# Kernel optimization log

Hardware: AMD Instinct MI355X
Metric: run time of the kernel (lower is better)

## Reference

```python
import jax, jax.numpy as jnp
import numpy as np

N, F, H, FO = 4096, 512, 4, 128  # nodes, in-feat, heads, out-feat per head
NEG_INF = -1e10
LRELU_ALPHA = 0.2


def setup_inputs() -> dict:
    key = jax.random.key(0)
    k_x, k_a, k_w, k_as, k_an = jax.random.split(key, 5)
    X = jax.random.normal(k_x, (N, F), dtype=jnp.float32)
    A = (jax.random.uniform(k_a, (N, N)) < 0.01).astype(jnp.float32)
    A = jnp.minimum(A + jnp.eye(N, dtype=jnp.float32), 1.0)
    W = jax.random.normal(k_w, (H, F, FO), dtype=jnp.float32) * 0.05       # per-head kernels
    b = jnp.zeros((H, FO), dtype=jnp.float32)                               # per-head biases
    a_self = jax.random.normal(k_as, (H, FO), dtype=jnp.float32) * 0.05    # attn_kernel_self (F_,1) per head
    a_neigh = jax.random.normal(k_an, (H, FO), dtype=jnp.float32) * 0.05   # attn_kernel_neigh (F_,1) per head
    return {"X": X, "A": A, "W": W, "b": b, "a_self": a_self, "a_neigh": a_neigh}


def reference(X, A, W, b, a_self, a_neigh):
    # features[h] = X @ W[h] -> [H, N, FO]
    feats = jnp.einsum('nf,hfo->hno', X, W)
    # Nx1 self / neighbor scores per head -> [H, N]
    e_s = jnp.einsum('hno,ho->hn', feats, a_self)
    e_n = jnp.einsum('hno,ho->hn', feats, a_neigh)
    # broadcast-add to [H, N, N], LeakyReLU(0.2), additive adjacency mask
    logits = e_s[:, :, None] + e_n[:, None, :]
    logits = jnp.where(logits > 0, logits, LRELU_ALPHA * logits)
    logits = logits + NEG_INF * (1.0 - A)[None, :, :]
    attn = jax.nn.softmax(logits, axis=-1)          # [H, N, N]
    out = jnp.einsum('hnm,hmo->hno', attn, feats)   # weighted aggregate
    out = out + b[:, None, :]
    # concat heads: [N, H*FO]
    out = jnp.transpose(out, (1, 0, 2)).reshape(X.shape[0], -1)
    return jax.nn.relu(out)
```

## Files before the change

kernel.cpp:

```cpp
#include <hip/hip_runtime.h>
#include <math.h>

#define NODES 4096
#define FIN   512
#define HEADS 4
#define FOUT  128
#define COLS  512

typedef short  short8  __attribute__((ext_vector_type(8)));
typedef float  floatx4 __attribute__((ext_vector_type(4)));

__device__ inline void split2(float x, short& hi, short& lo) {
    unsigned xb = __float_as_uint(x);
    unsigned hb = xb & 0xFFFF0000u;
    float hf = __uint_as_float(hb);
    float r  = x - hf;
    hi = (short)(hb >> 16);
    lo = (short)(__float_as_uint(r) >> 16);
}

__global__ __launch_bounds__(256) void convert_split(
    const float* __restrict__ X, const float* __restrict__ W,
    short* __restrict__ Xhi, short* __restrict__ Xlo,
    short* __restrict__ Wthi, short* __restrict__ Wtlo)
{
    int t = blockIdx.x * 256 + threadIdx.x;
    const int NX = NODES * FIN;
    const int stride = gridDim.x * 256;
    for (int i = t; i < NX; i += stride) {
        short hi, lo; split2(X[i], hi, lo);
        Xhi[i] = hi; Xlo[i] = lo;
    }
    const int NW = HEADS * FIN * FOUT;
    for (int i = t; i < NW; i += stride) {
        int h = i >> 16;
        int f = (i >> 7) & (FIN - 1);
        int o = i & (FOUT - 1);
        short hi, lo; split2(W[i], hi, lo);
        size_t dst = (size_t)(h * FOUT + o) * FIN + f;
        Wthi[dst] = hi; Wtlo[dst] = lo;
    }
}

__global__ __launch_bounds__(256) void gemm_mfma(
    const short* __restrict__ Xhi, const short* __restrict__ Xlo,
    const short* __restrict__ Bthi, const short* __restrict__ Btlo,
    float* __restrict__ feats)
{
    __shared__ short Ah[64][40], Al[64][40], Bh[64][40], Bl[64][40];
    const int tid = threadIdx.x;
    const int rowBase = blockIdx.y * 64;
    const int colBase = blockIdx.x * 64;
    const int lane = tid & 63, w = tid >> 6;
    const int quad = lane >> 4, lk = quad * 8, lm = lane & 15;

    floatx4 acc[4];
    #pragma unroll
    for (int mi = 0; mi < 4; mi++) acc[mi] = (floatx4)0.f;

    const int sr = tid >> 2;
    const int sk = (tid & 3) * 8;

    for (int k0 = 0; k0 < FIN; k0 += 32) {
        const float4 ah = *(const float4*)(Xhi  + (size_t)(rowBase + sr) * FIN + k0 + sk);
        const float4 al = *(const float4*)(Xlo  + (size_t)(rowBase + sr) * FIN + k0 + sk);
        const float4 bh = *(const float4*)(Bthi + (size_t)(colBase + sr) * FIN + k0 + sk);
        const float4 bl = *(const float4*)(Btlo + (size_t)(colBase + sr) * FIN + k0 + sk);
        __syncthreads();
        *(float4*)&Ah[sr][sk] = ah;
        *(float4*)&Al[sr][sk] = al;
        *(float4*)&Bh[sr][sk] = bh;
        *(float4*)&Bl[sr][sk] = bl;
        __syncthreads();

        short8 afh[4], afl[4];
        #pragma unroll
        for (int mi = 0; mi < 4; mi++) {
            afh[mi] = *(const short8*)&Ah[mi * 16 + lm][lk];
            afl[mi] = *(const short8*)&Al[mi * 16 + lm][lk];
        }
        short8 bfh = *(const short8*)&Bh[w * 16 + lm][lk];
        short8 bfl = *(const short8*)&Bl[w * 16 + lm][lk];
        #pragma unroll
        for (int mi = 0; mi < 4; mi++) {
            acc[mi] = __builtin_amdgcn_mfma_f32_16x16x32_bf16(afh[mi], bfh, acc[mi], 0, 0, 0);
            acc[mi] = __builtin_amdgcn_mfma_f32_16x16x32_bf16(afh[mi], bfl, acc[mi], 0, 0, 0);
            acc[mi] = __builtin_amdgcn_mfma_f32_16x16x32_bf16(afl[mi], bfh, acc[mi], 0, 0, 0);
        }
    }
    #pragma unroll
    for (int mi = 0; mi < 4; mi++) {
        #pragma unroll
        for (int r = 0; r < 4; r++) {
            int row = rowBase + mi * 16 + quad * 4 + r;
            int col = colBase + w * 16 + lm;
            feats[(size_t)row * COLS + col] = acc[mi][r];
        }
    }
}

__global__ __launch_bounds__(64) void scores(
    const float* __restrict__ feats, const float* __restrict__ a_self,
    const float* __restrict__ a_neigh, float* __restrict__ e_s, float* __restrict__ e_n)
{
    const int n = blockIdx.x;
    const int l = threadIdx.x;
    float ps[HEADS], pn[HEADS];
    #pragma unroll
    for (int hh = 0; hh < HEADS; hh++) {
        float x0 = feats[(size_t)n * COLS + hh * FOUT + l];
        float x1 = feats[(size_t)n * COLS + hh * FOUT + l + 64];
        ps[hh] = x0 * a_self[hh * FOUT + l]  + x1 * a_self[hh * FOUT + l + 64];
        pn[hh] = x0 * a_neigh[hh * FOUT + l] + x1 * a_neigh[hh * FOUT + l + 64];
    }
    #pragma unroll
    for (int off = 32; off > 0; off >>= 1) {
        #pragma unroll
        for (int hh = 0; hh < HEADS; hh++) {
            ps[hh] += __shfl_xor(ps[hh], off, 64);
            pn[hh] += __shfl_xor(pn[hh], off, 64);
        }
    }
    if (l == 0) {
        #pragma unroll
        for (int hh = 0; hh < HEADS; hh++) {
            e_s[hh * NODES + n] = ps[hh];
            e_n[hh * NODES + n] = pn[hh];
        }
    }
}

__global__ __launch_bounds__(256) void aggregate(
    const float* __restrict__ A, const float* __restrict__ feats,
    const float* __restrict__ e_s, const float* __restrict__ e_n,
    const float* __restrict__ bias, float* __restrict__ out)
{
    const int i = blockIdx.x;
    const int tid = threadIdx.x;
    __shared__ int   s_idx[NODES];
    __shared__ float s_w[HEADS][512];
    __shared__ int   s_cnt;
    __shared__ float s_dinv[HEADS];
    if (tid == 0) s_cnt = 0;
    __syncthreads();

    const float4* Arow = (const float4*)(A + (size_t)i * NODES);
    for (int q = tid; q < NODES / 4; q += 256) {
        float4 a = Arow[q];
        int j = q * 4;
        if (a.x != 0.f) s_idx[atomicAdd(&s_cnt, 1)] = j;
        if (a.y != 0.f) s_idx[atomicAdd(&s_cnt, 1)] = j + 1;
        if (a.z != 0.f) s_idx[atomicAdd(&s_cnt, 1)] = j + 2;
        if (a.w != 0.f) s_idx[atomicAdd(&s_cnt, 1)] = j + 3;
    }
    __syncthreads();
    const int cnt = s_cnt;

    const int wv = tid >> 6, lane = tid & 63;
    const float esi = e_s[wv * NODES + i];

    float m = -1e30f;
    for (int k = lane; k < cnt; k += 64) {
        float e = esi + e_n[wv * NODES + s_idx[k]];
        m = fmaxf(m, e > 0.f ? e : 0.2f * e);
    }
    #pragma unroll
    for (int off = 32; off > 0; off >>= 1) m = fmaxf(m, __shfl_xor(m, off, 64));

    const int c0 = tid, c1 = tid + 256;
    const int h0 = c0 >> 7, h1 = c1 >> 7;
    float acc0 = 0.f, acc1 = 0.f, d = 0.f;
    for (int base = 0; base < cnt; base += 512) {
        int nc = min(512, cnt - base);
        __syncthreads();
        for (int k = lane; k < nc; k += 64) {
            float e = esi + e_n[wv * NODES + s_idx[base + k]];
            float l = e > 0.f ? e : 0.2f * e;
            float wgt = __expf(l - m);
            s_w[wv][k] = wgt;
            d += wgt;
        }
        __syncthreads();
        for (int k = 0; k < nc; k++) {
            size_t off = (size_t)s_idx[base + k] * COLS;
            acc0 = fmaf(s_w[h0][k], feats[off + c0], acc0);
            acc1 = fmaf(s_w[h1][k], feats[off + c1], acc1);
        }
    }
    #pragma unroll
    for (int off = 32; off > 0; off >>= 1) d += __shfl_xor(d, off, 64);
    if (lane == 0) s_dinv[wv] = 1.f / d;
    __syncthreads();

    float o0 = acc0 * s_dinv[h0] + bias[h0 * FOUT + (c0 & 127)];
    float o1 = acc1 * s_dinv[h1] + bias[h1 * FOUT + (c1 & 127)];
    out[(size_t)i * COLS + c0] = fmaxf(o0, 0.f);
    out[(size_t)i * COLS + c1] = fmaxf(o1, 0.f);
}

extern "C" void kernel_launch(void* const* d_in, const int* in_sizes, int n_in,
                              void* d_out, int out_size, void* d_ws, size_t ws_size,
                              hipStream_t stream) {
    const float* X       = (const float*)d_in[0];
    const float* A       = (const float*)d_in[1];
    const float* W       = (const float*)d_in[2];
    const float* b       = (const float*)d_in[3];
    const float* a_self  = (const float*)d_in[4];
    const float* a_neigh = (const float*)d_in[5];
    float* out = (float*)d_out;

    float* feats = (float*)d_ws;
    float* e_s   = feats + (size_t)NODES * COLS;
    float* e_n   = e_s + HEADS * NODES;
    short* Xhi   = (short*)(e_n + HEADS * NODES);
    short* Xlo   = Xhi + (size_t)NODES * FIN;
    short* Wthi  = Xlo + (size_t)NODES * FIN;
    short* Wtlo  = Wthi + (size_t)COLS * FIN;

    convert_split<<<2048, 256, 0, stream>>>(X, W, Xhi, Xlo, Wthi, Wtlo);
    dim3 gA(COLS / 64, NODES / 64);
    gemm_mfma<<<gA, 256, 0, stream>>>(Xhi, Xlo, Wthi, Wtlo, feats);
    scores<<<NODES, 64, 0, stream>>>(feats, a_self, a_neigh, e_s, e_n);
    aggregate<<<NODES, 256, 0, stream>>>(A, feats, e_s, e_n, b, out);
}
```

Baseline: 162.4 us.

## Fuse X bf16 split into GEMM, double-buffer LDS, vectorize scores and aggregate

Removes the separate conversion pass over X: the GEMM now loads fp32 X and splits it into hi/lo bf16 in registers, and only W is pre-converted by a small kernel. The GEMM double-buffers LDS with register prefetch, which leaves one barrier per k-step. The scores kernel packs four nodes per block and uses float2 loads. Aggregate has each thread accumulate four columns with float4 gathers, splits neighbors across two halves of the block, and combines the partial sums through shared memory. The cost is more register pressure in the GEMM and an extra reduction step in aggregate.

```diff
diff --git a/kernel.cpp b/kernel.cpp
--- a/kernel.cpp
+++ b/kernel.cpp
@@ -10,77 +10,89 @@
 typedef short  short8  __attribute__((ext_vector_type(8)));
 typedef float  floatx4 __attribute__((ext_vector_type(4)));
 
-__device__ inline void split2(float x, short& hi, short& lo) {
-    unsigned xb = __float_as_uint(x);
-    unsigned hb = xb & 0xFFFF0000u;
-    float hf = __uint_as_float(hb);
-    float r  = x - hf;
-    hi = (short)(hb >> 16);
-    lo = (short)(__float_as_uint(r) >> 16);
-}
-
-__global__ __launch_bounds__(256) void convert_split(
-    const float* __restrict__ X, const float* __restrict__ W,
-    short* __restrict__ Xhi, short* __restrict__ Xlo,
-    short* __restrict__ Wthi, short* __restrict__ Wtlo)
+__device__ inline void split8(const float4& a, const float4& b, short8& hi, short8& lo) {
+    float v[8] = {a.x, a.y, a.z, a.w, b.x, b.y, b.z, b.w};
+    #pragma unroll
+    for (int i = 0; i < 8; i++) {
+        unsigned xb = __float_as_uint(v[i]);
+        unsigned hb = xb & 0xFFFF0000u;
+        hi[i] = (short)(hb >> 16);
+        float r = v[i] - __uint_as_float(hb);
+        lo[i] = (short)(__float_as_uint(r) >> 16);
+    }
+}
+
+__global__ __launch_bounds__(256) void convert_w(
+    const float* __restrict__ W, short* __restrict__ Wthi, short* __restrict__ Wtlo)
 {
     int t = blockIdx.x * 256 + threadIdx.x;
-    const int NX = NODES * FIN;
-    const int stride = gridDim.x * 256;
-    for (int i = t; i < NX; i += stride) {
-        short hi, lo; split2(X[i], hi, lo);
-        Xhi[i] = hi; Xlo[i] = lo;
-    }
-    const int NW = HEADS * FIN * FOUT;
-    for (int i = t; i < NW; i += stride) {
-        int h = i >> 16;
-        int f = (i >> 7) & (FIN - 1);
-        int o = i & (FOUT - 1);
-        short hi, lo; split2(W[i], hi, lo);
-        size_t dst = (size_t)(h * FOUT + o) * FIN + f;
-        Wthi[dst] = hi; Wtlo[dst] = lo;
-    }
+    int o = t & 127;
+    int hs = t >> 7;
+    int h = hs >> 6, seg = hs & 63;
+    float4 a, b;
+    float va[8];
+    #pragma unroll
+    for (int i = 0; i < 8; i++)
+        va[i] = W[((size_t)(h * FIN) + seg * 8 + i) * FOUT + o];
+    a = make_float4(va[0], va[1], va[2], va[3]);
+    b = make_float4(va[4], va[5], va[6], va[7]);
+    short8 hi, lo; split8(a, b, hi, lo);
+    size_t dst = (size_t)(h * FOUT + o) * FIN + seg * 8;
+    *(short8*)&Wthi[dst] = hi;
+    *(short8*)&Wtlo[dst] = lo;
 }
 
 __global__ __launch_bounds__(256) void gemm_mfma(
-    const short* __restrict__ Xhi, const short* __restrict__ Xlo,
+    const float* __restrict__ X,
     const short* __restrict__ Bthi, const short* __restrict__ Btlo,
     float* __restrict__ feats)
 {
-    __shared__ short Ah[64][40], Al[64][40], Bh[64][40], Bl[64][40];
+    __shared__ short Ah[2][64][40], Al[2][64][40], Bh[2][64][40], Bl[2][64][40];
     const int tid = threadIdx.x;
     const int rowBase = blockIdx.y * 64;
     const int colBase = blockIdx.x * 64;
     const int lane = tid & 63, w = tid >> 6;
     const int quad = lane >> 4, lk = quad * 8, lm = lane & 15;
-
-    floatx4 acc[4];
-    #pragma unroll
-    for (int mi = 0; mi < 4; mi++) acc[mi] = (floatx4)0.f;
-
     const int sr = tid >> 2;
     const int sk = (tid & 3) * 8;
 
-    for (int k0 = 0; k0 < FIN; k0 += 32) {
-        const float4 ah = *(const float4*)(Xhi  + (size_t)(rowBase + sr) * FIN + k0 + sk);
-        const float4 al = *(const float4*)(Xlo  + (size_t)(rowBase + sr) * FIN + k0 + sk);
-        const float4 bh = *(const float4*)(Bthi + (size_t)(colBase + sr) * FIN + k0 + sk);
-        const float4 bl = *(const float4*)(Btlo + (size_t)(colBase + sr) * FIN + k0 + sk);
+    const float* xp = X + (size_t)(rowBase + sr) * FIN + sk;
+    const short* bhp = Bthi + (size_t)(colBase + sr) * FIN + sk;
+    const short* blp = Btlo + (size_t)(colBase + sr) * FIN + sk;
+
+    floatx4 acc[4];
+    #pragma unroll
+    for (int mi = 0; mi < 4; mi++) acc[mi] = (floatx4)0.f;
+
+    float4 xa = *(const float4*)(xp);
+    float4 xb = *(const float4*)(xp + 4);
+    short8 rbh = *(const short8*)(bhp);
+    short8 rbl = *(const short8*)(blp);
+
+    for (int it = 0; it < FIN / 32; ++it) {
+        const int cur = it & 1;
+        short8 hi, lo; split8(xa, xb, hi, lo);
+        *(short8*)&Ah[cur][sr][sk] = hi;
+        *(short8*)&Al[cur][sr][sk] = lo;
+        *(short8*)&Bh[cur][sr][sk] = rbh;
+        *(short8*)&Bl[cur][sr][sk] = rbl;
+        if (it + 1 < FIN / 32) {
+            int k0 = (it + 1) * 32;
+            xa  = *(const float4*)(xp + k0);
+            xb  = *(const float4*)(xp + k0 + 4);
+            rbh = *(const short8*)(bhp + k0);
+            rbl = *(const short8*)(blp + k0);
+        }
         __syncthreads();
-        *(float4*)&Ah[sr][sk] = ah;
-        *(float4*)&Al[sr][sk] = al;
-        *(float4*)&Bh[sr][sk] = bh;
-        *(float4*)&Bl[sr][sk] = bl;
-        __syncthreads();
 
         short8 afh[4], afl[4];
         #pragma unroll
         for (int mi = 0; mi < 4; mi++) {
-            afh[mi] = *(const short8*)&Ah[mi * 16 + lm][lk];
-            afl[mi] = *(const short8*)&Al[mi * 16 + lm][lk];
-        }
-        short8 bfh = *(const short8*)&Bh[w * 16 + lm][lk];
-        short8 bfl = *(const short8*)&Bl[w * 16 + lm][lk];
+            afh[mi] = *(const short8*)&Ah[cur][mi * 16 + lm][lk];
+            afl[mi] = *(const short8*)&Al[cur][mi * 16 + lm][lk];
+        }
+        short8 bfh = *(const short8*)&Bh[cur][w * 16 + lm][lk];
+        short8 bfl = *(const short8*)&Bl[cur][w * 16 + lm][lk];
         #pragma unroll
         for (int mi = 0; mi < 4; mi++) {
             acc[mi] = __builtin_amdgcn_mfma_f32_16x16x32_bf16(afh[mi], bfh, acc[mi], 0, 0, 0);
@@ -99,33 +111,34 @@
     }
 }
 
-__global__ __launch_bounds__(64) void scores(
+__global__ __launch_bounds__(256) void scores(
     const float* __restrict__ feats, const float* __restrict__ a_self,
     const float* __restrict__ a_neigh, float* __restrict__ e_s, float* __restrict__ e_n)
 {
-    const int n = blockIdx.x;
-    const int l = threadIdx.x;
+    const int n = blockIdx.x * 4 + (threadIdx.x >> 6);
+    const int l = threadIdx.x & 63;
     float ps[HEADS], pn[HEADS];
     #pragma unroll
-    for (int hh = 0; hh < HEADS; hh++) {
-        float x0 = feats[(size_t)n * COLS + hh * FOUT + l];
-        float x1 = feats[(size_t)n * COLS + hh * FOUT + l + 64];
-        ps[hh] = x0 * a_self[hh * FOUT + l]  + x1 * a_self[hh * FOUT + l + 64];
-        pn[hh] = x0 * a_neigh[hh * FOUT + l] + x1 * a_neigh[hh * FOUT + l + 64];
+    for (int s = 0; s < HEADS; s++) {
+        float2 x  = *(const float2*)(feats + (size_t)n * COLS + s * FOUT + 2 * l);
+        float2 as = *(const float2*)(a_self  + s * FOUT + 2 * l);
+        float2 an = *(const float2*)(a_neigh + s * FOUT + 2 * l);
+        ps[s] = x.x * as.x + x.y * as.y;
+        pn[s] = x.x * an.x + x.y * an.y;
     }
     #pragma unroll
     for (int off = 32; off > 0; off >>= 1) {
         #pragma unroll
-        for (int hh = 0; hh < HEADS; hh++) {
-            ps[hh] += __shfl_xor(ps[hh], off, 64);
-            pn[hh] += __shfl_xor(pn[hh], off, 64);
+        for (int s = 0; s < HEADS; s++) {
+            ps[s] += __shfl_xor(ps[s], off, 64);
+            pn[s] += __shfl_xor(pn[s], off, 64);
         }
     }
     if (l == 0) {
         #pragma unroll
-        for (int hh = 0; hh < HEADS; hh++) {
-            e_s[hh * NODES + n] = ps[hh];
-            e_n[hh * NODES + n] = pn[hh];
+        for (int s = 0; s < HEADS; s++) {
+            e_s[s * NODES + n] = ps[s];
+            e_n[s * NODES + n] = pn[s];
         }
     }
 }
@@ -139,6 +152,7 @@
     const int tid = threadIdx.x;
     __shared__ int   s_idx[NODES];
     __shared__ float s_w[HEADS][512];
+    __shared__ float s_part[128][5];
     __shared__ int   s_cnt;
     __shared__ float s_dinv[HEADS];
     if (tid == 0) s_cnt = 0;
@@ -167,12 +181,13 @@
     #pragma unroll
     for (int off = 32; off > 0; off >>= 1) m = fmaxf(m, __shfl_xor(m, off, 64));
 
-    const int c0 = tid, c1 = tid + 256;
-    const int h0 = c0 >> 7, h1 = c1 >> 7;
-    float acc0 = 0.f, acc1 = 0.f, d = 0.f;
+    const int cg   = tid & 127;
+    const int half = tid >> 7;
+    const int h    = cg >> 5;
+    floatx4 acc = (floatx4)0.f;
+    float d = 0.f;
     for (int base = 0; base < cnt; base += 512) {
         int nc = min(512, cnt - base);
-        __syncthreads();
         for (int k = lane; k < nc; k += 64) {
             float e = esi + e_n[wv * NODES + s_idx[base + k]];
             float l = e > 0.f ? e : 0.2f * e;
@@ -181,21 +196,36 @@
             d += wgt;
         }
         __syncthreads();
-        for (int k = 0; k < nc; k++) {
-            size_t off = (size_t)s_idx[base + k] * COLS;
-            acc0 = fmaf(s_w[h0][k], feats[off + c0], acc0);
-            acc1 = fmaf(s_w[h1][k], feats[off + c1], acc1);
-        }
+        for (int k = half; k < nc; k += 2) {
+            int j = s_idx[base + k];
+            float wgt = s_w[h][k];
+            float4 f = *(const float4*)(feats + (size_t)j * COLS + cg * 4);
+            acc[0] = fmaf(wgt, f.x, acc[0]);
+            acc[1] = fmaf(wgt, f.y, acc[1]);
+            acc[2] = fmaf(wgt, f.z, acc[2]);
+            acc[3] = fmaf(wgt, f.w, acc[3]);
+        }
+        __syncthreads();
     }
     #pragma unroll
     for (int off = 32; off > 0; off >>= 1) d += __shfl_xor(d, off, 64);
     if (lane == 0) s_dinv[wv] = 1.f / d;
+
+    if (half == 1) {
+        s_part[cg][0] = acc[0]; s_part[cg][1] = acc[1];
+        s_part[cg][2] = acc[2]; s_part[cg][3] = acc[3];
+    }
     __syncthreads();
-
-    float o0 = acc0 * s_dinv[h0] + bias[h0 * FOUT + (c0 & 127)];
-    float o1 = acc1 * s_dinv[h1] + bias[h1 * FOUT + (c1 & 127)];
-    out[(size_t)i * COLS + c0] = fmaxf(o0, 0.f);
-    out[(size_t)i * COLS + c1] = fmaxf(o1, 0.f);
+    if (half == 0) {
+        float dinv = s_dinv[h];
+        float4 b4 = *(const float4*)(bias + h * FOUT + (cg & 31) * 4);
+        float o0 = (acc[0] + s_part[cg][0]) * dinv + b4.x;
+        float o1 = (acc[1] + s_part[cg][1]) * dinv + b4.y;
+        float o2 = (acc[2] + s_part[cg][2]) * dinv + b4.z;
+        float o3 = (acc[3] + s_part[cg][3]) * dinv + b4.w;
+        *(float4*)(out + (size_t)i * COLS + cg * 4) =
+            make_float4(fmaxf(o0, 0.f), fmaxf(o1, 0.f), fmaxf(o2, 0.f), fmaxf(o3, 0.f));
+    }
 }
 
 extern "C" void kernel_launch(void* const* d_in, const int* in_sizes, int n_in,
@@ -212,14 +242,12 @@
     float* feats = (float*)d_ws;
     float* e_s   = feats + (size_t)NODES * COLS;
     float* e_n   = e_s + HEADS * NODES;
-    short* Xhi   = (short*)(e_n + HEADS * NODES);
-    short* Xlo   = Xhi + (size_t)NODES * FIN;
-    short* Wthi  = Xlo + (size_t)NODES * FIN;
+    short* Wthi  = (short*)(e_n + HEADS * NODES);
     short* Wtlo  = Wthi + (size_t)COLS * FIN;
 
-    convert_split<<<2048, 256, 0, stream>>>(X, W, Xhi, Xlo, Wthi, Wtlo);
+    convert_w<<<128, 256, 0, stream>>>(W, Wthi, Wtlo);
     dim3 gA(COLS / 64, NODES / 64);
-    gemm_mfma<<<gA, 256, 0, stream>>>(Xhi, Xlo, Wthi, Wtlo, feats);
-    scores<<<NODES, 64, 0, stream>>>(feats, a_self, a_neigh, e_s, e_n);
+    gemm_mfma<<<gA, 256, 0, stream>>>(X, Wthi, Wtlo, feats);
+    scores<<<NODES / 4, 256, 0, stream>>>(feats, a_self, a_neigh, e_s, e_n);
     aggregate<<<NODES, 256, 0, stream>>>(A, feats, e_s, e_n, b, out);
 }
```

Result: slower. 166.6 us (+2.6%).
